# Kernel tuning notes

Hardware: AMD Instinct MI355X
Metric: run time of the kernel (lower is better)

## Reference

```python
import jax, jax.numpy as jnp
import numpy as np

B, S, D = 2, 2048, 1024
H = 16
HD = D // H  # 64
EPS = 1e-6
ROPE_BASE = 10000.0


def _rms_norm(x, w, eps=EPS):
    # torch nn.RMSNorm over last dim
    var = jnp.mean(jnp.square(x), axis=-1, keepdims=True)
    return x * jax.lax.rsqrt(var + eps) * w


def _rope_tables(seq_len, head_dim, base=ROPE_BASE):
    inv_freq = 1.0 / (base ** (jnp.arange(0, head_dim, 2, dtype=jnp.float32) / head_dim))
    t = jnp.arange(seq_len, dtype=jnp.float32)
    freqs = t[:, None] * inv_freq[None, :]            # [S, HD/2]
    emb = jnp.concatenate([freqs, freqs], axis=-1)    # [S, HD]
    return jnp.cos(emb), jnp.sin(emb)


def _rotate_half(x):
    x1, x2 = jnp.split(x, 2, axis=-1)
    return jnp.concatenate([-x2, x1], axis=-1)


def _apply_rope(x, cos, sin):
    # x: [B, H, S, HD]; cos/sin: [S, HD]
    return x * cos[None, None] + _rotate_half(x) * sin[None, None]


def setup_inputs() -> dict:
    key = jax.random.key(0)
    ks = jax.random.split(key, 8)
    scale = 1.0 / np.sqrt(D)
    return {
        "x": jax.random.normal(ks[0], (B, S, D), dtype=jnp.float32),
        "wq": jax.random.normal(ks[1], (D, D), dtype=jnp.float32) * scale,
        "wk": jax.random.normal(ks[2], (D, D), dtype=jnp.float32) * scale,
        "wv": jax.random.normal(ks[3], (D, D), dtype=jnp.float32) * scale,
        "wo": jax.random.normal(ks[4], (D, D), dtype=jnp.float32) * scale,
        "q_norm_w": jnp.ones((HD,), dtype=jnp.float32),
        "k_norm_w": jnp.ones((HD,), dtype=jnp.float32),
        "sink_logit": jnp.zeros((H,), dtype=jnp.float32),
    }


def reference(x, wq, wk, wv, wo, q_norm_w, k_norm_w, sink_logit):
    b, s, _ = x.shape
    # QKV projections (nn.Linear, no bias): y = x @ W^T
    q = jnp.einsum("bsd,od->bso", x, wq).reshape(b, s, H, HD)
    k = jnp.einsum("bsd,od->bso", x, wk).reshape(b, s, H, HD)
    v = jnp.einsum("bsd,od->bso", x, wv).reshape(b, s, H, HD)
    # QK RMSNorm (per head_dim)
    q = _rms_norm(q, q_norm_w)
    k = _rms_norm(k, k_norm_w)
    # [B, H, S, HD]
    q = q.transpose(0, 2, 1, 3)
    k = k.transpose(0, 2, 1, 3)
    v = v.transpose(0, 2, 1, 3)
    # full-head RoPE
    cos, sin = _rope_tables(s, HD)
    q = _apply_rope(q, cos, sin)
    k = _apply_rope(k, cos, sin)
    # manual attention with causal mask and sink softmax
    scale = HD ** -0.5
    scores = jnp.einsum("bhqd,bhkd->bhqk", q, k) * scale  # [B,H,S,S]
    causal = jnp.tril(jnp.ones((s, s), dtype=bool))
    scores = jnp.where(causal[None, None], scores, -jnp.inf)
    # sink-augmented softmax in fp32: append per-head sink logit, softmax, drop sink column
    sink = jnp.broadcast_to(sink_logit.astype(jnp.float32)[None, :, None, None], (b, H, s, 1))
    aug = jnp.concatenate([scores.astype(jnp.float32), sink], axis=-1)
    weights = jax.nn.softmax(aug, axis=-1)[..., :s].astype(scores.dtype)
    out = jnp.einsum("bhqk,bhkd->bhqd", weights, v)
    out = out.transpose(0, 2, 1, 3).reshape(b, s, D)
    return jnp.einsum("bsd,od->bso", out, wo)
```

## Files before the change

kernel.cpp:

```cpp
#include <hip/hip_runtime.h>

#define Bb 2
#define Ss 2048
#define Dd 1024
#define Hh 16
#define HDd 64
#define BS (Bb * Ss)

typedef __attribute__((ext_vector_type(8))) __bf16 bf16x8;
typedef __attribute__((ext_vector_type(4))) float f32x4;

__device__ __forceinline__ unsigned short f2bf(float f) {
  union { float f; unsigned u; } v; v.f = f;
  unsigned r = v.u + 0x7fffu + ((v.u >> 16) & 1u);
  return (unsigned short)(r >> 16);
}
__device__ __forceinline__ unsigned short f2bf_fast(float f) {
  union { float f; unsigned u; } v; v.f = f;
  return (unsigned short)((v.u + 0x8000u) >> 16);
}

__device__ __forceinline__ void gl_lds16(const void* g, void* l) {
  __builtin_amdgcn_global_load_lds(
      (const __attribute__((address_space(1))) void*)g,
      (__attribute__((address_space(3))) void*)l, 16, 0, 0);
}

__global__ __launch_bounds__(256) void cast_all(
    const float4* __restrict__ x, const float4* __restrict__ wq,
    const float4* __restrict__ wk, const float4* __restrict__ wv,
    const float4* __restrict__ wo, ushort4* __restrict__ xb,
    ushort4* __restrict__ wqkvb, ushort4* __restrict__ wob,
    float* __restrict__ ct, float* __restrict__ st) {
  int i = blockIdx.x * 256 + threadIdx.x;
  const int NX4 = BS * Dd / 4;
  const int NW4 = Dd * Dd / 4;
  const float4* src;
  ushort4* dst;
  int idx;
  if (i < NX4) { src = x; dst = xb; idx = i; }
  else if ((i -= NX4) < NW4) { src = wq; dst = wqkvb; idx = i; }
  else if ((i -= NW4) < NW4) { src = wk; dst = wqkvb + NW4; idx = i; }
  else if ((i -= NW4) < NW4) { src = wv; dst = wqkvb + 2 * NW4; idx = i; }
  else if ((i -= NW4) < NW4) { src = wo; dst = wob; idx = i; }
  else if ((i -= NW4) < Ss * 32) {
    int s = i >> 5, jj = i & 31;
    float freq = __powf(10000.0f, -(float)jj * (1.0f / 32.0f));
    float cs, sn;
    sincosf((float)s * freq, &sn, &cs);
    ct[i] = cs; st[i] = sn;
    return;
  } else return;
  float4 v = src[idx];
  ushort4 o;
  o.x = f2bf(v.x); o.y = f2bf(v.y); o.z = f2bf(v.z); o.w = f2bf(v.w);
  dst[idx] = o;
}

__global__ __launch_bounds__(256) void gemm_qkv(
    const unsigned short* __restrict__ A, const unsigned short* __restrict__ Bw,
    const float* __restrict__ qw, const float* __restrict__ kw,
    const float* __restrict__ ct, const float* __restrict__ st,
    unsigned short* __restrict__ Qb, unsigned short* __restrict__ Kb,
    unsigned short* __restrict__ Vt) {
  __shared__ __align__(16) unsigned short As[128 * 32];
  __shared__ __align__(16) unsigned short Bs[128 * 32];
  const int K = Dd, tid = threadIdx.x;
  const int lane = tid & 63;
  const int quad = lane >> 4;
  const int l16 = lane & 15;
  const int wave = tid >> 6;
  const int wm = (wave >> 1) * 64;
  const int wn = (wave & 1) * 64;
  const int tile_m = blockIdx.y * 128;
  const int tile_n = blockIdx.x * 128;

  const int off0 = tid * 16;
  const int off1 = 4096 + tid * 16;
  const int r0 = tid >> 2, r1 = r0 + 64;
  const int sch = (((tid & 3) ^ ((tid >> 3) & 3)) << 3);
  const int xg = ((quad ^ ((l16 >> 1) & 3)) << 3);

  const unsigned short* Ag0 = A + (size_t)(tile_m + r0) * K + sch;
  const unsigned short* Ag1 = A + (size_t)(tile_m + r1) * K + sch;
  const unsigned short* Bg0 = Bw + (size_t)(tile_n + r0) * K + sch;
  const unsigned short* Bg1 = Bw + (size_t)(tile_n + r1) * K + sch;

  f32x4 zero = {0.f, 0.f, 0.f, 0.f};
  f32x4 acc[4][4];
#pragma unroll
  for (int mi = 0; mi < 4; ++mi)
#pragma unroll
    for (int ni = 0; ni < 4; ++ni) acc[mi][ni] = zero;

  for (int k0 = 0; k0 < K; k0 += 32) {
    gl_lds16(Ag0 + k0, (char*)As + off0);
    gl_lds16(Ag1 + k0, (char*)As + off1);
    gl_lds16(Bg0 + k0, (char*)Bs + off0);
    gl_lds16(Bg1 + k0, (char*)Bs + off1);
    __syncthreads();
    bf16x8 af[4], bfv[4];
#pragma unroll
    for (int mi = 0; mi < 4; ++mi)
      af[mi] = *(const bf16x8*)&As[(wm + mi * 16 + l16) * 32 + xg];
#pragma unroll
    for (int ni = 0; ni < 4; ++ni)
      bfv[ni] = *(const bf16x8*)&Bs[(wn + ni * 16 + l16) * 32 + xg];
#pragma unroll
    for (int mi = 0; mi < 4; ++mi)
#pragma unroll
      for (int ni = 0; ni < 4; ++ni)
        acc[mi][ni] = __builtin_amdgcn_mfma_f32_16x16x32_bf16(
            af[mi], bfv[ni], acc[mi][ni], 0, 0, 0);
    __syncthreads();
  }

  const int type = blockIdx.x >> 3;
  const int h = (((blockIdx.x & 7) << 7) + wn) >> 6;
  const int bb = tile_m >> 11;
  const size_t bh = (size_t)bb * Hh + h;

  if (type == 2) {
#pragma unroll
    for (int mi = 0; mi < 4; ++mi) {
      int s0 = (tile_m + wm + mi * 16 + quad * 4) & (Ss - 1);
#pragma unroll
      for (int ni = 0; ni < 4; ++ni) {
        int d = ni * 16 + l16;
        ushort4 pv;
        pv.x = f2bf(acc[mi][ni][0]);
        pv.y = f2bf(acc[mi][ni][1]);
        pv.z = f2bf(acc[mi][ni][2]);
        pv.w = f2bf(acc[mi][ni][3]);
        *(ushort4*)&Vt[(bh * HDd + d) * Ss + s0] = pv;
      }
    }
  } else {
    const float* wnp = type ? kw : qw;
    unsigned short* Ob = type ? Kb : Qb;
    const float fscale = type ? 1.0f : 0.125f * 1.44269504f;
    float w0[4];
#pragma unroll
    for (int ni = 0; ni < 4; ++ni) w0[ni] = wnp[ni * 16 + l16];
#pragma unroll
    for (int mi = 0; mi < 4; ++mi) {
#pragma unroll
      for (int r = 0; r < 4; ++r) {
        int s = (tile_m + wm + mi * 16 + quad * 4 + r) & (Ss - 1);
        float ss2 = 0.f;
#pragma unroll
        for (int ni = 0; ni < 4; ++ni) ss2 += acc[mi][ni][r] * acc[mi][ni][r];
        ss2 += __shfl_xor(ss2, 1, 64);
        ss2 += __shfl_xor(ss2, 2, 64);
        ss2 += __shfl_xor(ss2, 4, 64);
        ss2 += __shfl_xor(ss2, 8, 64);
        float rr = rsqrtf(ss2 * (1.0f / 64.0f) + 1e-6f) * fscale;
        float c0 = ct[s * 32 + l16], c1 = ct[s * 32 + 16 + l16];
        float sn0 = st[s * 32 + l16], sn1 = st[s * 32 + 16 + l16];
#pragma unroll
        for (int ni = 0; ni < 4; ++ni) {
          float vn = acc[mi][ni][r] * rr * w0[ni];
          float vp = acc[mi][ni ^ 2][r] * rr * w0[ni ^ 2];
          float cs_ = (ni & 1) ? c1 : c0;
          float sn_ = (ni & 1) ? sn1 : sn0;
          float sg = (ni < 2) ? -1.0f : 1.0f;
          Ob[(bh * Ss + s) * HDd + ni * 16 + l16] = f2bf(vn * cs_ + sg * vp * sn_);
        }
      }
    }
  }
}

__global__ __launch_bounds__(256) void gemm_bt2(
    const unsigned short* __restrict__ A, const unsigned short* __restrict__ Bw,
    float* __restrict__ C, int M, int N, int K) {
  __shared__ __align__(16) unsigned short As[128 * 32];
  __shared__ __align__(16) unsigned short Bs[64 * 32];
  const int tid = threadIdx.x;
  const int lane = tid & 63;
  const int quad = lane >> 4;
  const int l16 = lane & 15;
  const int wave = tid >> 6;
  const int wm = (wave >> 1) * 64;
  const int wn = (wave & 1) * 32;
  const int tile_m = blockIdx.y * 128;
  const int tile_n = blockIdx.x * 64;

  const int off0 = tid * 16;
  const int off1 = 4096 + tid * 16;
  const int r0 = tid >> 2, r1 = r0 + 64;
  const int sch = (((tid & 3) ^ ((tid >> 3) & 3)) << 3);
  const int xg = ((quad ^ ((l16 >> 1) & 3)) << 3);

  const unsigned short* Ag0 = A + (size_t)(tile_m + r0) * K + sch;
  const unsigned short* Ag1 = A + (size_t)(tile_m + r1) * K + sch;
  const unsigned short* Bg0 = Bw + (size_t)(tile_n + r0) * K + sch;

  f32x4 zero = {0.f, 0.f, 0.f, 0.f};
  f32x4 acc[4][2];
#pragma unroll
  for (int mi = 0; mi < 4; ++mi)
#pragma unroll
    for (int ni = 0; ni < 2; ++ni) acc[mi][ni] = zero;

  for (int k0 = 0; k0 < K; k0 += 32) {
    gl_lds16(Ag0 + k0, (char*)As + off0);
    gl_lds16(Ag1 + k0, (char*)As + off1);
    gl_lds16(Bg0 + k0, (char*)Bs + off0);
    __syncthreads();
    bf16x8 af[4], bfv[2];
#pragma unroll
    for (int mi = 0; mi < 4; ++mi)
      af[mi] = *(const bf16x8*)&As[(wm + mi * 16 + l16) * 32 + xg];
#pragma unroll
    for (int ni = 0; ni < 2; ++ni)
      bfv[ni] = *(const bf16x8*)&Bs[(wn + ni * 16 + l16) * 32 + xg];
#pragma unroll
    for (int mi = 0; mi < 4; ++mi)
#pragma unroll
      for (int ni = 0; ni < 2; ++ni)
        acc[mi][ni] = __builtin_amdgcn_mfma_f32_16x16x32_bf16(
            af[mi], bfv[ni], acc[mi][ni], 0, 0, 0);
    __syncthreads();
  }

#pragma unroll
  for (int mi = 0; mi < 4; ++mi) {
#pragma unroll
    for (int ni = 0; ni < 2; ++ni) {
      int col = tile_n + wn + ni * 16 + l16;
#pragma unroll
      for (int r = 0; r < 4; ++r) {
        int row = tile_m + wm + mi * 16 + quad * 4 + r;
        C[(size_t)row * N + col] = acc[mi][ni][r];
      }
    }
  }
}

__global__ __launch_bounds__(256) void flash(
    const unsigned short* __restrict__ Qb, const unsigned short* __restrict__ Kb,
    const unsigned short* __restrict__ Vt, const float* __restrict__ sink,
    unsigned short* __restrict__ Ob) {
  __shared__ __align__(16) unsigned short Qs[64 * 64];
  __shared__ __align__(16) unsigned short Ks[2][64 * 64];
  __shared__ __align__(16) unsigned short Vs[2][64 * 64];
  __shared__ __align__(16) unsigned short Ps[4][16 * 72];

  int tid = threadIdx.x, lane = tid & 63, wave = tid >> 6;
  int quad = lane >> 4, l16 = lane & 15;
  int bx = blockIdx.x;
  int h = blockIdx.y, b = blockIdx.z;

  const unsigned short* Qg = Qb + ((size_t)(b * Hh + h) * Ss) * HDd;
  const unsigned short* Kg = Kb + ((size_t)(b * Hh + h) * Ss) * HDd;
  const unsigned short* Vg = Vt + ((size_t)(b * Hh + h) * HDd) * Ss;

  int off0 = tid * 16, off1 = 4096 + tid * 16;
  int sr0 = tid >> 3, sr1 = sr0 + 32;
  int sch = ((tid & 7) ^ (sr0 & 7)) * 8;
  int x0 = ((quad ^ (l16 & 7)) * 8);
  int x1 = x0 ^ 32;

  float sk = sink[h];
  f32x4 zero = {0.f, 0.f, 0.f, 0.f};

#pragma unroll 1
  for (int pass = 0; pass < 2; ++pass) {
    int qt = pass ? bx : 31 - bx;
    int q0 = qt * 64;
    int myq = q0 + wave * 16 + l16;

    __syncthreads();
    gl_lds16(Qg + (size_t)(q0 + sr0) * 64 + sch, (char*)Qs + off0);
    gl_lds16(Qg + (size_t)(q0 + sr1) * 64 + sch, (char*)Qs + off1);
    gl_lds16(Kg + (size_t)sr0 * 64 + sch, (char*)Ks[0] + off0);
    gl_lds16(Kg + (size_t)sr1 * 64 + sch, (char*)Ks[0] + off1);
    gl_lds16(Vg + (size_t)sr0 * Ss + sch, (char*)Vs[0] + off0);
    gl_lds16(Vg + (size_t)sr1 * Ss + sch, (char*)Vs[0] + off1);

    float l_part = 0.f;
    f32x4 Oacc[4];
#pragma unroll
    for (int ni = 0; ni < 4; ++ni) Oacc[ni] = zero;
    bf16x8 aq0, aq1;

    for (int kt = 0; kt <= qt; ++kt) {
      __syncthreads();
      if (kt == 0) {
        aq0 = *(const bf16x8*)&Qs[(wave * 16 + l16) * 64 + x0];
        aq1 = *(const bf16x8*)&Qs[(wave * 16 + l16) * 64 + x1];
      }
      const unsigned short* Kt = Ks[kt & 1];
      const unsigned short* Vtile = Vs[kt & 1];
      int nxt = kt + 1;
      if (nxt <= qt) {
        gl_lds16(Kg + (size_t)(nxt * 64 + sr0) * 64 + sch, (char*)Ks[nxt & 1] + off0);
        gl_lds16(Kg + (size_t)(nxt * 64 + sr1) * 64 + sch, (char*)Ks[nxt & 1] + off1);
        gl_lds16(Vg + (size_t)sr0 * Ss + nxt * 64 + sch, (char*)Vs[nxt & 1] + off0);
        gl_lds16(Vg + (size_t)sr1 * Ss + nxt * 64 + sch, (char*)Vs[nxt & 1] + off1);
      }

      f32x4 sc[4];
#pragma unroll
      for (int ni = 0; ni < 4; ++ni) {
        bf16x8 bk0 = *(const bf16x8*)&Kt[(ni * 16 + l16) * 64 + x0];
        bf16x8 bk1 = *(const bf16x8*)&Kt[(ni * 16 + l16) * 64 + x1];
        sc[ni] = __builtin_amdgcn_mfma_f32_16x16x32_bf16(bk0, aq0, zero, 0, 0, 0);
        sc[ni] = __builtin_amdgcn_mfma_f32_16x16x32_bf16(bk1, aq1, sc[ni], 0, 0, 0);
      }

      if (kt == qt) {
#pragma unroll
        for (int ni = 0; ni < 4; ++ni)
#pragma unroll
          for (int r = 0; r < 4; ++r)
            if (kt * 64 + ni * 16 + quad * 4 + r > myq) sc[ni][r] = -1.0e38f;
      }

#pragma unroll
      for (int ni = 0; ni < 4; ++ni) {
        float p0 = exp2f(sc[ni][0]);
        float p1 = exp2f(sc[ni][1]);
        float p2 = exp2f(sc[ni][2]);
        float p3 = exp2f(sc[ni][3]);
        l_part += (p0 + p1) + (p2 + p3);
        ushort4 pk;
        pk.x = f2bf_fast(p0);
        pk.y = f2bf_fast(p1);
        pk.z = f2bf_fast(p2);
        pk.w = f2bf_fast(p3);
        *(ushort4*)&Ps[wave][l16 * 72 + ni * 16 + quad * 4] = pk;
      }

      asm volatile("s_waitcnt lgkmcnt(0)" ::: "memory");
      bf16x8 ap0 = *(const bf16x8*)&Ps[wave][l16 * 72 + quad * 8];
      bf16x8 ap1 = *(const bf16x8*)&Ps[wave][l16 * 72 + 32 + quad * 8];

#pragma unroll
      for (int ni = 0; ni < 4; ++ni) {
        bf16x8 bv0 = *(const bf16x8*)&Vtile[(ni * 16 + l16) * 64 + x0];
        bf16x8 bv1 = *(const bf16x8*)&Vtile[(ni * 16 + l16) * 64 + x1];
        Oacc[ni] = __builtin_amdgcn_mfma_f32_16x16x32_bf16(bv0, ap0, Oacc[ni], 0, 0, 0);
        Oacc[ni] = __builtin_amdgcn_mfma_f32_16x16x32_bf16(bv1, ap1, Oacc[ni], 0, 0, 0);
      }
    }

    l_part += __shfl_xor(l_part, 16, 64);
    l_part += __shfl_xor(l_part, 32, 64);
    float inv = 1.0f / (l_part + __expf(sk));
#pragma unroll
    for (int ni = 0; ni < 4; ++ni) {
      ushort4 ov;
      ov.x = f2bf(Oacc[ni][0] * inv);
      ov.y = f2bf(Oacc[ni][1] * inv);
      ov.z = f2bf(Oacc[ni][2] * inv);
      ov.w = f2bf(Oacc[ni][3] * inv);
      *(ushort4*)&Ob[((size_t)b * Ss + myq) * Dd + h * 64 + ni * 16 + quad * 4] = ov;
    }
  }
}

extern "C" void kernel_launch(void* const* d_in, const int* in_sizes, int n_in,
                              void* d_out, int out_size, void* d_ws, size_t ws_size,
                              hipStream_t stream) {
  const float* x  = (const float*)d_in[0];
  const float* wq = (const float*)d_in[1];
  const float* wk = (const float*)d_in[2];
  const float* wv = (const float*)d_in[3];
  const float* wo = (const float*)d_in[4];
  const float* qw = (const float*)d_in[5];
  const float* kw = (const float*)d_in[6];
  const float* sk = (const float*)d_in[7];

  char* ws = (char*)d_ws;
  const size_t MB = 1ull << 20;
  unsigned short* xb    = (unsigned short*)(ws + 0);
  unsigned short* attnb = (unsigned short*)(ws + 0);
  unsigned short* wqkvb = (unsigned short*)(ws + 8 * MB);
  unsigned short* wob   = (unsigned short*)(ws + 14 * MB);
  float*          ct    = (float*)(ws + 16 * MB);
  float*          st    = (float*)(ws + 17 * MB);
  unsigned short* Qb    = (unsigned short*)(ws + 40 * MB);
  unsigned short* Kb    = (unsigned short*)(ws + 48 * MB);
  unsigned short* Vt    = (unsigned short*)(ws + 56 * MB);

  cast_all<<<8448, 256, 0, stream>>>(
      (const float4*)x, (const float4*)wq, (const float4*)wk, (const float4*)wv,
      (const float4*)wo, (ushort4*)xb, (ushort4*)wqkvb, (ushort4*)wob, ct, st);
  gemm_qkv<<<dim3(24, 32), 256, 0, stream>>>(xb, wqkvb, qw, kw, ct, st, Qb, Kb, Vt);
  flash<<<dim3(16, Hh, Bb), 256, 0, stream>>>(Qb, Kb, Vt, sk, attnb);
  gemm_bt2<<<dim3(16, 32), 256, 0, stream>>>(attnb, wob, (float*)d_out, BS, Dd, Dd);
}
```

Before: 206.4 us.

## Software-pipeline QK^T one tile ahead, triple-buffer V, row-sum via MFMA

Restructures the flash-attention inner loop so the QK^T scores for the next key tile are computed while the current tile's probabilities are being exponentiated and multiplied by V. K tiles are prefetched two steps ahead and V uses a triple buffer, and the final-iteration barrier is skipped. The softmax denominator is now taken from an extra MFMA against a ones vector instead of scalar adds and shuffles, so it sums the bf16-rounded probabilities. This aims to hide LDS and exp latency behind matrix work, at the cost of more registers and LDS.

```diff
diff --git a/kernel.cpp b/kernel.cpp
--- a/kernel.cpp
+++ b/kernel.cpp
@@ -8,6 +8,7 @@
 #define BS (Bb * Ss)
 
 typedef __attribute__((ext_vector_type(8))) __bf16 bf16x8;
+typedef __attribute__((ext_vector_type(8))) unsigned short u16x8;
 typedef __attribute__((ext_vector_type(4))) float f32x4;
 
 __device__ __forceinline__ unsigned short f2bf(float f) {
@@ -244,7 +245,7 @@
     unsigned short* __restrict__ Ob) {
   __shared__ __align__(16) unsigned short Qs[64 * 64];
   __shared__ __align__(16) unsigned short Ks[2][64 * 64];
-  __shared__ __align__(16) unsigned short Vs[2][64 * 64];
+  __shared__ __align__(16) unsigned short Vs[3][64 * 64];
   __shared__ __align__(16) unsigned short Ps[4][16 * 72];
 
   int tid = threadIdx.x, lane = tid & 63, wave = tid >> 6;
@@ -264,6 +265,14 @@
 
   float sk = sink[h];
   f32x4 zero = {0.f, 0.f, 0.f, 0.f};
+
+  bf16x8 ones;
+  {
+    u16x8 t;
+#pragma unroll
+    for (int i = 0; i < 8; ++i) t[i] = 0x3F80;
+    ones = *(bf16x8*)&t;
+  }
 
 #pragma unroll 1
   for (int pass = 0; pass < 2; ++pass) {
@@ -279,64 +288,81 @@
     gl_lds16(Vg + (size_t)sr0 * Ss + sch, (char*)Vs[0] + off0);
     gl_lds16(Vg + (size_t)sr1 * Ss + sch, (char*)Vs[0] + off1);
 
-    float l_part = 0.f;
-    f32x4 Oacc[4];
+    f32x4 Oacc[4], lacc = zero;
 #pragma unroll
     for (int ni = 0; ni < 4; ++ni) Oacc[ni] = zero;
-    bf16x8 aq0, aq1;
+
+    __syncthreads();
+    bf16x8 aq0 = *(const bf16x8*)&Qs[(wave * 16 + l16) * 64 + x0];
+    bf16x8 aq1 = *(const bf16x8*)&Qs[(wave * 16 + l16) * 64 + x1];
+    if (qt >= 1) {
+      gl_lds16(Kg + (size_t)(64 + sr0) * 64 + sch, (char*)Ks[1] + off0);
+      gl_lds16(Kg + (size_t)(64 + sr1) * 64 + sch, (char*)Ks[1] + off1);
+      gl_lds16(Vg + (size_t)sr0 * Ss + 64 + sch, (char*)Vs[1] + off0);
+      gl_lds16(Vg + (size_t)sr1 * Ss + 64 + sch, (char*)Vs[1] + off1);
+    }
+
+    f32x4 sc[4];
+#pragma unroll
+    for (int ni = 0; ni < 4; ++ni) {
+      bf16x8 bk0 = *(const bf16x8*)&Ks[0][(ni * 16 + l16) * 64 + x0];
+      bf16x8 bk1 = *(const bf16x8*)&Ks[0][(ni * 16 + l16) * 64 + x1];
+      sc[ni] = __builtin_amdgcn_mfma_f32_16x16x32_bf16(bk0, aq0, zero, 0, 0, 0);
+      sc[ni] = __builtin_amdgcn_mfma_f32_16x16x32_bf16(bk1, aq1, sc[ni], 0, 0, 0);
+    }
+    if (qt == 0) {
+#pragma unroll
+      for (int ni = 0; ni < 4; ++ni)
+#pragma unroll
+        for (int r = 0; r < 4; ++r)
+          if (ni * 16 + quad * 4 + r > myq - q0) sc[ni][r] = -1.0e38f;
+    }
 
     for (int kt = 0; kt <= qt; ++kt) {
-      __syncthreads();
-      if (kt == 0) {
-        aq0 = *(const bf16x8*)&Qs[(wave * 16 + l16) * 64 + x0];
-        aq1 = *(const bf16x8*)&Qs[(wave * 16 + l16) * 64 + x1];
-      }
-      const unsigned short* Kt = Ks[kt & 1];
-      const unsigned short* Vtile = Vs[kt & 1];
-      int nxt = kt + 1;
-      if (nxt <= qt) {
-        gl_lds16(Kg + (size_t)(nxt * 64 + sr0) * 64 + sch, (char*)Ks[nxt & 1] + off0);
-        gl_lds16(Kg + (size_t)(nxt * 64 + sr1) * 64 + sch, (char*)Ks[nxt & 1] + off1);
-        gl_lds16(Vg + (size_t)sr0 * Ss + nxt * 64 + sch, (char*)Vs[nxt & 1] + off0);
-        gl_lds16(Vg + (size_t)sr1 * Ss + nxt * 64 + sch, (char*)Vs[nxt & 1] + off1);
-      }
-
-      f32x4 sc[4];
+      bool last = (kt == qt);
+      if (!last) __syncthreads();
+      if (kt + 2 <= qt) {
+        int vb = (kt + 2) % 3, kb = kt & 1;
+        gl_lds16(Kg + (size_t)((kt + 2) * 64 + sr0) * 64 + sch, (char*)Ks[kb] + off0);
+        gl_lds16(Kg + (size_t)((kt + 2) * 64 + sr1) * 64 + sch, (char*)Ks[kb] + off1);
+        gl_lds16(Vg + (size_t)sr0 * Ss + (kt + 2) * 64 + sch, (char*)Vs[vb] + off0);
+        gl_lds16(Vg + (size_t)sr1 * Ss + (kt + 2) * 64 + sch, (char*)Vs[vb] + off1);
+      }
+
 #pragma unroll
       for (int ni = 0; ni < 4; ++ni) {
-        bf16x8 bk0 = *(const bf16x8*)&Kt[(ni * 16 + l16) * 64 + x0];
-        bf16x8 bk1 = *(const bf16x8*)&Kt[(ni * 16 + l16) * 64 + x1];
-        sc[ni] = __builtin_amdgcn_mfma_f32_16x16x32_bf16(bk0, aq0, zero, 0, 0, 0);
-        sc[ni] = __builtin_amdgcn_mfma_f32_16x16x32_bf16(bk1, aq1, sc[ni], 0, 0, 0);
-      }
-
-      if (kt == qt) {
-#pragma unroll
-        for (int ni = 0; ni < 4; ++ni)
-#pragma unroll
-          for (int r = 0; r < 4; ++r)
-            if (kt * 64 + ni * 16 + quad * 4 + r > myq) sc[ni][r] = -1.0e38f;
-      }
-
-#pragma unroll
-      for (int ni = 0; ni < 4; ++ni) {
-        float p0 = exp2f(sc[ni][0]);
-        float p1 = exp2f(sc[ni][1]);
-        float p2 = exp2f(sc[ni][2]);
-        float p3 = exp2f(sc[ni][3]);
-        l_part += (p0 + p1) + (p2 + p3);
         ushort4 pk;
-        pk.x = f2bf_fast(p0);
-        pk.y = f2bf_fast(p1);
-        pk.z = f2bf_fast(p2);
-        pk.w = f2bf_fast(p3);
+        pk.x = f2bf_fast(exp2f(sc[ni][0]));
+        pk.y = f2bf_fast(exp2f(sc[ni][1]));
+        pk.z = f2bf_fast(exp2f(sc[ni][2]));
+        pk.w = f2bf_fast(exp2f(sc[ni][3]));
         *(ushort4*)&Ps[wave][l16 * 72 + ni * 16 + quad * 4] = pk;
+      }
+
+      f32x4 scn[4];
+      if (!last) {
+        const unsigned short* Kt = Ks[(kt + 1) & 1];
+#pragma unroll
+        for (int ni = 0; ni < 4; ++ni) {
+          bf16x8 bk0 = *(const bf16x8*)&Kt[(ni * 16 + l16) * 64 + x0];
+          bf16x8 bk1 = *(const bf16x8*)&Kt[(ni * 16 + l16) * 64 + x1];
+          scn[ni] = __builtin_amdgcn_mfma_f32_16x16x32_bf16(bk0, aq0, zero, 0, 0, 0);
+          scn[ni] = __builtin_amdgcn_mfma_f32_16x16x32_bf16(bk1, aq1, scn[ni], 0, 0, 0);
+        }
+        if (kt + 1 == qt) {
+#pragma unroll
+          for (int ni = 0; ni < 4; ++ni)
+#pragma unroll
+            for (int r = 0; r < 4; ++r)
+              if ((kt + 1) * 64 + ni * 16 + quad * 4 + r > myq) scn[ni][r] = -1.0e38f;
+        }
       }
 
       asm volatile("s_waitcnt lgkmcnt(0)" ::: "memory");
       bf16x8 ap0 = *(const bf16x8*)&Ps[wave][l16 * 72 + quad * 8];
       bf16x8 ap1 = *(const bf16x8*)&Ps[wave][l16 * 72 + 32 + quad * 8];
 
+      const unsigned short* Vtile = Vs[kt % 3];
 #pragma unroll
       for (int ni = 0; ni < 4; ++ni) {
         bf16x8 bv0 = *(const bf16x8*)&Vtile[(ni * 16 + l16) * 64 + x0];
@@ -344,11 +370,16 @@
         Oacc[ni] = __builtin_amdgcn_mfma_f32_16x16x32_bf16(bv0, ap0, Oacc[ni], 0, 0, 0);
         Oacc[ni] = __builtin_amdgcn_mfma_f32_16x16x32_bf16(bv1, ap1, Oacc[ni], 0, 0, 0);
       }
-    }
-
-    l_part += __shfl_xor(l_part, 16, 64);
-    l_part += __shfl_xor(l_part, 32, 64);
-    float inv = 1.0f / (l_part + __expf(sk));
+      lacc = __builtin_amdgcn_mfma_f32_16x16x32_bf16(ones, ap0, lacc, 0, 0, 0);
+      lacc = __builtin_amdgcn_mfma_f32_16x16x32_bf16(ones, ap1, lacc, 0, 0, 0);
+
+      if (!last) {
+#pragma unroll
+        for (int ni = 0; ni < 4; ++ni) sc[ni] = scn[ni];
+      }
+    }
+
+    float inv = 1.0f / (lacc[0] + exp2f(sk * 1.44269504f));
 #pragma unroll
     for (int ni = 0; ni < 4; ++ni) {
       ushort4 ov;
```

Result: faster. 201.5 us (-2.4%).
